# Kernel optimization log

Hardware: AMD Instinct MI355X
Metric: run time of the kernel (lower is better)

The kernel has to match this reference:

```python
import jax, jax.numpy as jnp
import numpy as np

K = 512
D = 64
N = 262144


def setup_inputs() -> dict:
    key = jax.random.key(0)
    k1, k2 = jax.random.split(key)
    z_e_x = jax.random.normal(k1, (N, D), dtype=jnp.float32)
    # nn.Embedding(K, D) with uniform_(-1/K, 1/K)
    codebook = jax.random.uniform(k2, (K, D), dtype=jnp.float32,
                                  minval=-1.0 / K, maxval=1.0 / K)
    return {"z_e_x": z_e_x, "codebook": codebook}


def _vq_indices(x_flat, codebook):
    c_sqr = jnp.sum(codebook * codebook, axis=1)          # [K]
    x_sqr = jnp.sum(x_flat * x_flat, axis=1, keepdims=True)  # [N,1]
    distances = x_sqr + c_sqr - 2.0 * (x_flat @ codebook.T)  # [N,K]
    return jnp.argmin(distances, axis=1)                  # [N] int


def reference(z_e_x, codebook):
    # VQEmbedding.straight_through with inactive_count=None
    x_flat = z_e_x.reshape(-1, codebook.shape[1])
    indices = _vq_indices(x_flat, codebook)
    # z_q_x: lookup into detached codebook
    z_q_x = codebook[indices].reshape(z_e_x.shape)
    # z_q_x_bar: lookup into live codebook (same values in fwd)
    z_q_x_bar = codebook[indices].reshape(z_e_x.shape)
    return z_q_x, z_q_x_bar, indices
```

## Files before the change

kernel.cpp:

```cpp
#include <hip/hip_runtime.h>
#include <math.h>

#define KCODES 512
#define DDIM   64
#define NROWS  262144
#define ND     ((size_t)NROWS * DDIM)
#define MBLK   64
#define CAP    8
#define MARGIN_HALF 7.5e-5f


typedef __attribute__((ext_vector_type(8))) short s16x8;
typedef __attribute__((ext_vector_type(4))) float f32x4;
union U4S8 { uint4 u; s16x8 s; };

__device__ __forceinline__ unsigned short bf16_rne(float f) {
    unsigned u = __float_as_uint(f);
    return (unsigned short)((u + 0x7FFFu + ((u >> 16) & 1u)) >> 16);
}
__device__ __forceinline__ float bf16_tof(unsigned short h) {
    return __uint_as_float(((unsigned)h) << 16);
}
__device__ __forceinline__ unsigned cvtpk_bf16(float a, float b) {
    unsigned r;
    asm("v_cvt_pk_bf16_f32 %0, %1, %2" : "=v"(r) : "v"(a), "v"(b));
    return r;
}

__device__ __forceinline__ void g2lds16(const void* g, void* l) {
    __builtin_amdgcn_global_load_lds(
        (const __attribute__((address_space(1))) unsigned int*)g,
        (__attribute__((address_space(3))) unsigned int*)l,
        16, 0, 0);
}

__device__ __forceinline__ float np_sumsq64(const float* v) {
    float r[8];
#pragma unroll
    for (int j = 0; j < 8; ++j) r[j] = __fmul_rn(v[j], v[j]);
#pragma unroll
    for (int i = 8; i < 64; i += 8) {
#pragma unroll
        for (int j = 0; j < 8; ++j)
            r[j] = __fadd_rn(r[j], __fmul_rn(v[i + j], v[i + j]));
    }
    float t01 = __fadd_rn(r[0], r[1]);
    float t23 = __fadd_rn(r[2], r[3]);
    float t45 = __fadd_rn(r[4], r[5]);
    float t67 = __fadd_rn(r[6], r[7]);
    return __fadd_rn(__fadd_rn(t01, t23), __fadd_rn(t45, t67));
}

__device__ __forceinline__ float np_xs_stream(const float4* __restrict__ xr) {
    float4 u = xr[0], w = xr[1];
    float r0 = __fmul_rn(u.x, u.x), r1 = __fmul_rn(u.y, u.y);
    float r2 = __fmul_rn(u.z, u.z), r3 = __fmul_rn(u.w, u.w);
    float r4 = __fmul_rn(w.x, w.x), r5 = __fmul_rn(w.y, w.y);
    float r6 = __fmul_rn(w.z, w.z), r7 = __fmul_rn(w.w, w.w);
#pragma unroll
    for (int i = 1; i < 8; ++i) {
        u = xr[2 * i]; w = xr[2 * i + 1];
        r0 = __fadd_rn(r0, __fmul_rn(u.x, u.x));
        r1 = __fadd_rn(r1, __fmul_rn(u.y, u.y));
        r2 = __fadd_rn(r2, __fmul_rn(u.z, u.z));
        r3 = __fadd_rn(r3, __fmul_rn(u.w, u.w));
        r4 = __fadd_rn(r4, __fmul_rn(w.x, w.x));
        r5 = __fadd_rn(r5, __fmul_rn(w.y, w.y));
        r6 = __fadd_rn(r6, __fmul_rn(w.z, w.z));
        r7 = __fadd_rn(r7, __fmul_rn(w.w, w.w));
    }
    float t01 = __fadd_rn(r0, r1), t23 = __fadd_rn(r2, r3);
    float t45 = __fadd_rn(r4, r5), t67 = __fadd_rn(r6, r7);
    return __fadd_rn(__fadd_rn(t01, t23), __fadd_rn(t45, t67));
}

__device__ __forceinline__ float dot_seq(const float4* __restrict__ xr,
                                         const float* __restrict__ c) {
    const float4* c4 = (const float4*)c;
    float a = 0.f;
#pragma unroll
    for (int i = 0; i < 16; ++i) {
        float4 xv = xr[i];
        float4 cv = c4[i];
        a = __fmaf_rn(xv.x, cv.x, a);
        a = __fmaf_rn(xv.y, cv.y, a);
        a = __fmaf_rn(xv.z, cv.z, a);
        a = __fmaf_rn(xv.w, cv.w, a);
    }
    return a;
}

__device__ __forceinline__ unsigned pair_pack(float va, float vb, int lo) {
    unsigned short ha = bf16_rne(va), hb = bf16_rne(vb);
    if (lo) {
        ha = bf16_rne(va - bf16_tof(ha));
        hb = bf16_rne(vb - bf16_tof(hb));
    }
    return (unsigned)ha | ((unsigned)hb << 16);
}

__global__ void vq_prep(const float* __restrict__ cb, float* __restrict__ cs,
                        float* __restrict__ csh, unsigned short* __restrict__ FR) {
    int bid = blockIdx.x, t = threadIdx.x;
    if (bid < 32) {
        int g = bid * 256 + t;
        int lane = g & 63, fr = (g >> 6) & 3, tt = (g >> 8) & 7, p = g >> 11;
        int mm = lane & 15, quad = lane >> 4;
        int k = p * 128 + tt * 16 + mm;
        int d0 = (fr & 1) * 32 + quad * 8;
        int lo = fr >> 1;
        const float* src = cb + (size_t)k * DDIM + d0;
        float4 a = *(const float4*)src;
        float4 b = *(const float4*)(src + 4);
        uint4 pk;
        pk.x = pair_pack(a.x, a.y, lo);
        pk.y = pair_pack(a.z, a.w, lo);
        pk.z = pair_pack(b.x, b.y, lo);
        pk.w = pair_pack(b.z, b.w, lo);
        ((uint4*)FR)[g] = pk;
    } else {
        int k = (bid - 32) * 256 + t;
        if (k < KCODES) {
            float v[DDIM];
            const float4* c4 = (const float4*)(cb + (size_t)k * DDIM);
#pragma unroll
            for (int i = 0; i < DDIM / 4; ++i) {
                float4 tv = c4[i];
                v[4 * i + 0] = tv.x; v[4 * i + 1] = tv.y;
                v[4 * i + 2] = tv.z; v[4 * i + 3] = tv.w;
            }
            float s = np_sumsq64(v);
            cs[k] = s;
            csh[k] = -0.5f * s;
        }
    }
}

__device__ __forceinline__ void pack8(float4 a, float4 b, uint4& hi, uint4& lo) {
    hi.x = cvtpk_bf16(a.x, a.y);
    hi.y = cvtpk_bf16(a.z, a.w);
    hi.z = cvtpk_bf16(b.x, b.y);
    hi.w = cvtpk_bf16(b.z, b.w);
    float r0 = a.x - __uint_as_float(hi.x << 16);
    float r1 = a.y - __uint_as_float(hi.x & 0xffff0000u);
    float r2 = a.z - __uint_as_float(hi.y << 16);
    float r3 = a.w - __uint_as_float(hi.y & 0xffff0000u);
    float r4 = b.x - __uint_as_float(hi.z << 16);
    float r5 = b.y - __uint_as_float(hi.z & 0xffff0000u);
    float r6 = b.z - __uint_as_float(hi.w << 16);
    float r7 = b.w - __uint_as_float(hi.w & 0xffff0000u);
    lo.x = cvtpk_bf16(r0, r1);
    lo.y = cvtpk_bf16(r2, r3);
    lo.z = cvtpk_bf16(r4, r5);
    lo.w = cvtpk_bf16(r6, r7);
}

#define SMEM_BYTES 37376

__launch_bounds__(256, 4)
__global__ void vq_main(const float* __restrict__ x, const float* __restrict__ cb,
                        const float* __restrict__ cs, const float* __restrict__ csh,
                        const unsigned short* __restrict__ FR,
                        float* __restrict__ out) {
    extern __shared__ char smem[];
    uint4* SB   = (uint4*)(smem);
    int*   cnt  = (int*)  (smem + 32768);
    int*   lstk = (int*)  (smem + 33024);
    float* lsts = (float*)(smem + 35072);
    int*   win  = (int*)  (smem + 37120);

    const int t    = threadIdx.x;
    const int ln   = t & 63;
    const int wv   = t >> 6;
    const int m    = ln & 15;
    const int quad = ln >> 4;
    const int rowBlk0 = blockIdx.x * MBLK;

    {
        const char* gsrc = (const char*)FR;
#pragma unroll
        for (int i = 0; i < 8; ++i)
            g2lds16(gsrc + (size_t)(i * 256 + wv * 64 + ln) * 16,
                    (char*)SB + (size_t)(i * 256 + wv * 64) * 16);
    }

    if (t < 64) cnt[t] = 0;

    const float* xrow = x + (size_t)(rowBlk0 + wv * 16 + m) * DDIM + quad * 8;
    U4S8 axh0, axh1, axl0, axl1;
    {
        float4 a0 = *(const float4*)(xrow);
        float4 b0 = *(const float4*)(xrow + 4);
        float4 a1 = *(const float4*)(xrow + 32);
        float4 b1 = *(const float4*)(xrow + 36);
        pack8(a0, b0, axh0.u, axl0.u);
        pack8(a1, b1, axh1.u, axl1.u);
    }

    float rm[4] = {-INFINITY, -INFINITY, -INFINITY, -INFINITY};

    for (int p = 0; p < 4; ++p) {
        __syncthreads();

        float chv[8];
#pragma unroll
        for (int tt = 0; tt < 8; ++tt) chv[tt] = csh[p * 128 + tt * 16 + m];

        float s[4][8];
#pragma unroll
        for (int tt = 0; tt < 8; ++tt) {
            U4S8 bh0, bh1, bl0, bl1;
            bh0.u = SB[(tt * 4 + 0) * 64 + ln];
            bh1.u = SB[(tt * 4 + 1) * 64 + ln];
            bl0.u = SB[(tt * 4 + 2) * 64 + ln];
            bl1.u = SB[(tt * 4 + 3) * 64 + ln];
            float ch = chv[tt];
            f32x4 acc = {ch, ch, ch, ch};
            acc = __builtin_amdgcn_mfma_f32_16x16x32_bf16(axh0.s, bh0.s, acc, 0, 0, 0);
            acc = __builtin_amdgcn_mfma_f32_16x16x32_bf16(axh1.s, bh1.s, acc, 0, 0, 0);
            acc = __builtin_amdgcn_mfma_f32_16x16x32_bf16(axl0.s, bh0.s, acc, 0, 0, 0);
            acc = __builtin_amdgcn_mfma_f32_16x16x32_bf16(axl1.s, bh1.s, acc, 0, 0, 0);
            acc = __builtin_amdgcn_mfma_f32_16x16x32_bf16(axh0.s, bl0.s, acc, 0, 0, 0);
            acc = __builtin_amdgcn_mfma_f32_16x16x32_bf16(axh1.s, bl1.s, acc, 0, 0, 0);
#pragma unroll
            for (int r = 0; r < 4; ++r)
                s[r][tt] = acc[r];
        }

        __syncthreads();

        if (p < 3) {
            const char* gsrc = (const char*)FR + (size_t)(p + 1) * 32768;
#pragma unroll
            for (int i = 0; i < 8; ++i)
                g2lds16(gsrc + (size_t)(i * 256 + wv * 64 + ln) * 16,
                        (char*)SB + (size_t)(i * 256 + wv * 64) * 16);
        }

#pragma unroll
        for (int r = 0; r < 4; ++r) {
            float mx = s[r][0];
#pragma unroll
            for (int tt = 1; tt < 8; ++tt) mx = fmaxf(mx, s[r][tt]);
            mx = fmaxf(mx, __shfl_xor(mx, 1, 64));
            mx = fmaxf(mx, __shfl_xor(mx, 2, 64));
            mx = fmaxf(mx, __shfl_xor(mx, 4, 64));
            mx = fmaxf(mx, __shfl_xor(mx, 8, 64));
            rm[r] = fmaxf(rm[r], mx);
        }
#pragma unroll
        for (int r = 0; r < 4; ++r) {
            float thr = rm[r] - MARGIN_HALF;
            int lrow = wv * 16 + quad * 4 + r;
#pragma unroll
            for (int tt = 0; tt < 8; ++tt) {
                if (s[r][tt] >= thr) {
                    int pos = atomicAdd(&cnt[lrow], 1);
                    if (pos < CAP) {
                        lstk[lrow * CAP + pos] = p * 128 + tt * 16 + m;
                        lsts[lrow * CAP + pos] = s[r][tt];
                    }
                }
            }
        }
    }

    __syncthreads();

    if (m < 4) {
        int lrow = wv * 16 + quad * 4 + m;
        float rmf = (m == 0) ? rm[0] : (m == 1) ? rm[1] : (m == 2) ? rm[2] : rm[3];
        float thr = rmf - MARGIN_HALF;
        int c = cnt[lrow];
        int kb;
        const float4* xr = (const float4*)(x + (size_t)(rowBlk0 + lrow) * DDIM);
        if (c <= CAP) {
            int nc = 0, k1 = 0;
            for (int i = 0; i < c; ++i)
                if (lsts[lrow * CAP + i] >= thr) { ++nc; k1 = lstk[lrow * CAP + i]; }
            if (nc == 1) {
                kb = k1;
            } else {
                float xs = np_xs_stream(xr);
                float db = INFINITY; kb = 0x7fffffff;
                for (int i = 0; i < c; ++i) {
                    if (lsts[lrow * CAP + i] >= thr) {
                        int k = lstk[lrow * CAP + i];
                        float a = dot_seq(xr, cb + (size_t)k * DDIM);
                        float d = __fadd_rn(__fadd_rn(xs, cs[k]), __fmul_rn(-2.0f, a));
                        if (d < db || (d == db && k < kb)) { db = d; kb = k; }
                    }
                }
            }
        } else {
            float xs = np_xs_stream(xr);
            float db = INFINITY; kb = 0;
            for (int k = 0; k < KCODES; ++k) {
                float a = dot_seq(xr, cb + (size_t)k * DDIM);
                float d = __fadd_rn(__fadd_rn(xs, cs[k]), __fmul_rn(-2.0f, a));
                if (d < db) { db = d; kb = k; }
            }
        }
        win[lrow] = kb;
        out[2 * ND + (size_t)(rowBlk0 + lrow)] = (float)kb;
    }
    __syncthreads();

#pragma unroll
    for (int i = 0; i < 4; ++i) {
        int g   = t + i * 256;
        int row = g >> 4, cc = g & 15;
        int kb  = win[row];
        float4 v = *(const float4*)(cb + (size_t)kb * DDIM + cc * 4);
        size_t gr = (size_t)(rowBlk0 + row) * DDIM + (size_t)cc * 4;
        *(float4*)(out + gr) = v;
        *(float4*)(out + ND + gr) = v;
    }
}

extern "C" void kernel_launch(void* const* d_in, const int* in_sizes, int n_in,
                              void* d_out, int out_size, void* d_ws, size_t ws_size,
                              hipStream_t stream) {
    const float* z  = (const float*)d_in[0];
    const float* cb = (const float*)d_in[1];
    float* out = (float*)d_out;
    float* cs          = (float*)d_ws;
    float* csh         = (float*)((char*)d_ws + 2048);
    unsigned short* FR = (unsigned short*)((char*)d_ws + 4096);

    (void)hipFuncSetAttribute((const void*)vq_main,
                              hipFuncAttributeMaxDynamicSharedMemorySize,
                              SMEM_BYTES);
    vq_prep<<<34, 256, 0, stream>>>(cb, cs, csh, FR);
    vq_main<<<NROWS / MBLK, 256, SMEM_BYTES, stream>>>(z, cb, cs, csh, FR, out);
}
```

Before: 236.4 us.

## Read codebook fragments directly from global and drop block barriers

Removes the LDS staging of the pre-packed bf16 codebook fragments. Each wave now loads its B operands straight from global memory, which is expected to hit in L1/L2 because every block reads the same 128 KB. Since each wave now touches only its own 16 rows' counters, candidate lists and winners, all __syncthreads are replaced by per-wave LDS waitcnt fences. LDS use drops to about 4.6 KB, which could raise occupancy. The cost is that every wave redundantly pulls the full fragment set through the cache hierarchy, and the global loads now sit on the MFMA critical path without prefetch overlap.

New measurement: 265.9 us. +12.5%, slower.

```diff
diff --git a/kernel.cpp b/kernel.cpp
--- a/kernel.cpp
+++ b/kernel.cpp
@@ -27,11 +27,9 @@
     return r;
 }
 
-__device__ __forceinline__ void g2lds16(const void* g, void* l) {
-    __builtin_amdgcn_global_load_lds(
-        (const __attribute__((address_space(1))) unsigned int*)g,
-        (__attribute__((address_space(3))) unsigned int*)l,
-        16, 0, 0);
+__device__ __forceinline__ void wave_fence_lds() {
+    asm volatile("s_waitcnt lgkmcnt(0)" ::: "memory");
+    __builtin_amdgcn_sched_barrier(0);
 }
 
 __device__ __forceinline__ float np_sumsq64(const float* v) {
@@ -155,7 +153,7 @@
     lo.w = cvtpk_bf16(r6, r7);
 }
 
-#define SMEM_BYTES 37376
+#define SMEM_BYTES 4608
 
 __launch_bounds__(256, 4)
 __global__ void vq_main(const float* __restrict__ x, const float* __restrict__ cb,
@@ -163,11 +161,10 @@
                         const unsigned short* __restrict__ FR,
                         float* __restrict__ out) {
     extern __shared__ char smem[];
-    uint4* SB   = (uint4*)(smem);
-    int*   cnt  = (int*)  (smem + 32768);
-    int*   lstk = (int*)  (smem + 33024);
-    float* lsts = (float*)(smem + 35072);
-    int*   win  = (int*)  (smem + 37120);
+    int*   cnt  = (int*)  (smem);
+    int*   lstk = (int*)  (smem + 256);
+    float* lsts = (float*)(smem + 2304);
+    int*   win  = (int*)  (smem + 4352);
 
     const int t    = threadIdx.x;
     const int ln   = t & 63;
@@ -176,15 +173,7 @@
     const int quad = ln >> 4;
     const int rowBlk0 = blockIdx.x * MBLK;
 
-    {
-        const char* gsrc = (const char*)FR;
-#pragma unroll
-        for (int i = 0; i < 8; ++i)
-            g2lds16(gsrc + (size_t)(i * 256 + wv * 64 + ln) * 16,
-                    (char*)SB + (size_t)(i * 256 + wv * 64) * 16);
-    }
-
-    if (t < 64) cnt[t] = 0;
+    if (ln < 16) cnt[wv * 16 + ln] = 0;
 
     const float* xrow = x + (size_t)(rowBlk0 + wv * 16 + m) * DDIM + quad * 8;
     U4S8 axh0, axh1, axl0, axl1;
@@ -198,10 +187,9 @@
     }
 
     float rm[4] = {-INFINITY, -INFINITY, -INFINITY, -INFINITY};
+    const uint4* FRg = (const uint4*)FR;
 
     for (int p = 0; p < 4; ++p) {
-        __syncthreads();
-
         float chv[8];
 #pragma unroll
         for (int tt = 0; tt < 8; ++tt) chv[tt] = csh[p * 128 + tt * 16 + m];
@@ -209,11 +197,12 @@
         float s[4][8];
 #pragma unroll
         for (int tt = 0; tt < 8; ++tt) {
+            const uint4* gB = FRg + (size_t)((p * 8 + tt) * 4) * 64 + ln;
             U4S8 bh0, bh1, bl0, bl1;
-            bh0.u = SB[(tt * 4 + 0) * 64 + ln];
-            bh1.u = SB[(tt * 4 + 1) * 64 + ln];
-            bl0.u = SB[(tt * 4 + 2) * 64 + ln];
-            bl1.u = SB[(tt * 4 + 3) * 64 + ln];
+            bh0.u = gB[0];
+            bh1.u = gB[64];
+            bl0.u = gB[128];
+            bl1.u = gB[192];
             float ch = chv[tt];
             f32x4 acc = {ch, ch, ch, ch};
             acc = __builtin_amdgcn_mfma_f32_16x16x32_bf16(axh0.s, bh0.s, acc, 0, 0, 0);
@@ -225,16 +214,6 @@
 #pragma unroll
             for (int r = 0; r < 4; ++r)
                 s[r][tt] = acc[r];
-        }
-
-        __syncthreads();
-
-        if (p < 3) {
-            const char* gsrc = (const char*)FR + (size_t)(p + 1) * 32768;
-#pragma unroll
-            for (int i = 0; i < 8; ++i)
-                g2lds16(gsrc + (size_t)(i * 256 + wv * 64 + ln) * 16,
-                        (char*)SB + (size_t)(i * 256 + wv * 64) * 16);
         }
 
 #pragma unroll
@@ -265,7 +244,7 @@
         }
     }
 
-    __syncthreads();
+    wave_fence_lds();
 
     if (m < 4) {
         int lrow = wv * 16 + quad * 4 + m;
@@ -304,12 +283,13 @@
         win[lrow] = kb;
         out[2 * ND + (size_t)(rowBlk0 + lrow)] = (float)kb;
     }
-    __syncthreads();
+
+    wave_fence_lds();
 
 #pragma unroll
     for (int i = 0; i < 4; ++i) {
-        int g   = t + i * 256;
-        int row = g >> 4, cc = g & 15;
+        int g   = i * 64 + ln;
+        int row = wv * 16 + (g >> 4), cc = g & 15;
         int kb  = win[row];
         float4 v = *(const float4*)(cb + (size_t)kb * DDIM + cc * 4);
         size_t gr = (size_t)(rowBlk0 + row) * DDIM + (size_t)cc * 4;
```
